# Kernel tuning notes

Hardware: AMD Instinct MI355X
Metric: run time of the kernel (lower is better)

## Reference

```python
import jax, jax.numpy as jnp
import numpy as np

N, NFEAT, NHID, NCLASS, NHEADS = 50000, 512, 256, 64, 8
C1 = NHID // NHEADS  # 32 per-head channels, layer 1
NEG_SLOPE = 0.2


def setup_inputs() -> dict:
    key = jax.random.key(0)
    ks = jax.random.split(key, 10)
    x = jax.random.normal(ks[0], (N, NFEAT), dtype=jnp.float32)
    edge_idx = jax.random.randint(ks[1], (2, 800000), 0, N, dtype=jnp.int64)
    s = 0.05
    return {
        "x": x,
        "edge_idx": edge_idx,
        "W1": jax.random.normal(ks[2], (NFEAT, NHEADS, C1), dtype=jnp.float32) * s,
        "a1_src": jax.random.normal(ks[3], (NHEADS, C1), dtype=jnp.float32) * s,
        "a1_dst": jax.random.normal(ks[4], (NHEADS, C1), dtype=jnp.float32) * s,
        "b1": jnp.zeros((NHID,), dtype=jnp.float32),
        "W2": jax.random.normal(ks[5], (NHID, NHEADS, NCLASS), dtype=jnp.float32) * s,
        "a2_src": jax.random.normal(ks[6], (NHEADS, NCLASS), dtype=jnp.float32) * s,
        "a2_dst": jax.random.normal(ks[7], (NHEADS, NCLASS), dtype=jnp.float32) * s,
        "b2": jnp.zeros((NCLASS,), dtype=jnp.float32),
    }


def gat_conv(x, src, dst, W, a_src, a_dst, b, concat):
    # x: [N, F_in]; W: [F_in, H, C]; a_*: [H, C]; src/dst: [E]
    h = jnp.einsum("nf,fhc->nhc", x, W)             # [N, H, C]
    e_src = jnp.sum(h * a_src, axis=-1)              # [N, H]
    e_dst = jnp.sum(h * a_dst, axis=-1)              # [N, H]
    alpha = e_src[src] + e_dst[dst]                  # [E, H]
    alpha = jnp.where(alpha > 0, alpha, NEG_SLOPE * alpha)  # leaky_relu(0.2)
    # segment softmax over incoming edges of each destination node
    m = jax.ops.segment_max(alpha, dst, num_segments=N)     # [N, H]
    m = jnp.where(jnp.isfinite(m), m, 0.0)
    e = jnp.exp(alpha - m[dst])                      # [E, H]
    z = jax.ops.segment_sum(e, dst, num_segments=N)  # [N, H]
    coef = e / z[dst]                                # [E, H]
    msg = h[src] * coef[:, :, None]                  # [E, H, C]
    out = jax.ops.segment_sum(msg, dst, num_segments=N)  # [N, H, C]
    if concat:
        out = out.reshape(N, -1)
    else:
        out = out.mean(axis=1)
    return out + b


def reference(x, edge_idx, W1, a1_src, a1_dst, b1, W2, a2_src, a2_dst, b2):
    # add self loops (PyG GATConv default)
    loop = jnp.arange(N, dtype=edge_idx.dtype)
    src = jnp.concatenate([edge_idx[0], loop])
    dst = jnp.concatenate([edge_idx[1], loop])
    h = gat_conv(x, src, dst, W1, a1_src, a1_dst, b1, concat=True)   # [N, NHID]
    h = jax.nn.relu(h)
    # dropout inactive (eval mode)
    out = gat_conv(h, src, dst, W2, a2_src, a2_dst, b2, concat=False)  # [N, NCLASS]
    return jax.nn.log_softmax(out, axis=1)
```

## Files before the change

kernel.cpp:

```cpp
#include <hip/hip_runtime.h>
#include <math.h>

#define NN 50000
#define NF 512
#define NHID 256
#define NCLASS 64
#define NHEADS 8

typedef __attribute__((ext_vector_type(8))) short bf16x8;
typedef __attribute__((ext_vector_type(4))) float f32x4;
typedef __attribute__((ext_vector_type(4))) unsigned int u32x4;
typedef __attribute__((ext_vector_type(2))) unsigned int u32x2;

static __device__ __forceinline__ unsigned short f2bf(float f) {
  unsigned int u = __float_as_uint(f);
  unsigned int r = (u + 0x7fffu + ((u >> 16) & 1u)) >> 16;
  return (unsigned short)r;
}
static __device__ __forceinline__ float bf2f(unsigned short u) {
  return __uint_as_float(((unsigned int)u) << 16);
}
static __device__ __forceinline__ float2 bfpair(unsigned int u) {
  return make_float2(__uint_as_float(u << 16), __uint_as_float(u & 0xffff0000u));
}

static __device__ __forceinline__ u32x4 gld128(const void* p) {
  u32x4 r;
  asm volatile("global_load_dwordx4 %0, %1, off"
               : "=v"(r) : "v"((unsigned long long)p));
  return r;
}
static __device__ __forceinline__ u32x2 gld64(const void* p) {
  u32x2 r;
  asm volatile("global_load_dwordx2 %0, %1, off"
               : "=v"(r) : "v"((unsigned long long)p));
  return r;
}
static __device__ __forceinline__ int gld32i(const void* p) {
  int r;
  asm volatile("global_load_dword %0, %1, off"
               : "=v"(r) : "v"((unsigned long long)p));
  return r;
}
static __device__ __forceinline__ float gld32f(const void* p) {
  float r;
  asm volatile("global_load_dword %0, %1, off"
               : "=v"(r) : "v"((unsigned long long)p));
  return r;
}
#define VMCNT0()                                        \
  do {                                                  \
    asm volatile("s_waitcnt vmcnt(0)" ::: "memory");    \
    __builtin_amdgcn_sched_barrier(0);                  \
  } while (0)

__global__ void k_init_deg(int* deg) {
  int i = blockIdx.x * blockDim.x + threadIdx.x;
  if (i < NN) deg[i] = 1;
}

__global__ void k_count(const int* __restrict__ dst, int E0, int* deg) {
  int i = blockIdx.x * blockDim.x + threadIdx.x;
  if (i < E0) atomicAdd(&deg[dst[i]], 1);
}

__global__ __launch_bounds__(1024) void k_scan(const int* __restrict__ deg, int* offs,
                                               int* cursor) {
  __shared__ int wbase[16];
  __shared__ int srun;
  int tid = threadIdx.x;
  int lane = tid & 63;
  int wv = tid >> 6;
  if (tid == 0) srun = 0;
  __syncthreads();
  for (int base = 0; base < NN; base += 4096) {
    int i = base + tid * 4;
    int4 v;
    if (i + 3 < NN) {
      v = *(const int4*)(deg + i);
    } else {
      v.x = (i + 0 < NN) ? deg[i + 0] : 0;
      v.y = (i + 1 < NN) ? deg[i + 1] : 0;
      v.z = (i + 2 < NN) ? deg[i + 2] : 0;
      v.w = (i + 3 < NN) ? deg[i + 3] : 0;
    }
    int tot = v.x + v.y + v.z + v.w;
    int s = tot;
    #pragma unroll
    for (int o = 1; o < 64; o <<= 1) {
      int t = __shfl_up(s, o);
      if (lane >= o) s += t;
    }
    if (lane == 63) wbase[wv] = s;
    __syncthreads();
    if (tid == 0) {
      int run = srun;
      #pragma unroll
      for (int w2 = 0; w2 < 16; w2++) {
        int t = wbase[w2];
        wbase[w2] = run;
        run += t;
      }
      srun = run;
    }
    __syncthreads();
    int p = wbase[wv] + s - tot;
    if (i + 0 < NN) { offs[i + 0] = p; cursor[i + 0] = p; p += v.x; }
    if (i + 1 < NN) { offs[i + 1] = p; cursor[i + 1] = p; p += v.y; }
    if (i + 2 < NN) { offs[i + 2] = p; cursor[i + 2] = p; p += v.z; }
    if (i + 3 < NN) { offs[i + 3] = p; cursor[i + 3] = p; }
  }
  __syncthreads();
  if (tid == 0) offs[NN] = srun;
}

__global__ void k_scatter(const int* __restrict__ src, const int* __restrict__ dst,
                          int E0, int* cursor, int* __restrict__ nbr) {
  int i = blockIdx.x * blockDim.x + threadIdx.x;
  if (i < E0) {
    int pos = atomicAdd(&cursor[dst[i]], 1);
    nbr[pos] = src[i];
  } else if (i < E0 + NN) {
    int v = i - E0;
    int pos = atomicAdd(&cursor[v], 1);
    nbr[pos] = v;
  }
}

__global__ void k_cast4(const float* __restrict__ in, unsigned short* __restrict__ out,
                        int n4) {
  int i = blockIdx.x * blockDim.x + threadIdx.x;
  if (i >= n4) return;
  float4 v = *(const float4*)(in + (size_t)i * 4);
  ushort4 o;
  o.x = f2bf(v.x); o.y = f2bf(v.y); o.z = f2bf(v.z); o.w = f2bf(v.w);
  *(ushort4*)(out + (size_t)i * 4) = o;
}

__global__ void k_castWt(const float* __restrict__ W, unsigned short* __restrict__ Wt,
                         int K, int cols) {
  int i = blockIdx.x * blockDim.x + threadIdx.x;
  if (i >= K * cols) return;
  int k = i / cols, c = i % cols;
  Wt[(size_t)c * K + k] = f2bf(W[i]);
}

__global__ void k_castWt_perm(const float* __restrict__ W, unsigned short* __restrict__ Wt,
                              int K) {
  int i = blockIdx.x * blockDim.x + threadIdx.x;
  if (i >= K * NHEADS * NCLASS) return;
  int k = i / (NHEADS * NCLASS);
  int rem = i % (NHEADS * NCLASS);
  int h = rem / NCLASS, c = rem % NCLASS;
  Wt[(size_t)(c * NHEADS + h) * K + k] = f2bf(W[i]);
}

__global__ __launch_bounds__(256) void k_gemm_bf(const unsigned short* __restrict__ A,
                                                 const unsigned short* __restrict__ Bt,
                                                 unsigned short* __restrict__ C,
                                                 int rows, int K, int cols) {
  __shared__ unsigned short Bs[256 * 40];
  int t = threadIdx.x;
  int wave = t >> 6, lane = t & 63;
  int quad = lane >> 4, sixt = lane & 15;
  int rb = blockIdx.x * 64 + (wave >> 1) * 32;
  int cw = (wave & 1) * 128;
  int cbw = blockIdx.y * 256 + cw;
  int r0 = rb + sixt, r1 = rb + 16 + sixt;
  const unsigned short* Ap0 = A + (size_t)(r0 < rows ? r0 : 0) * K + quad * 8;
  const unsigned short* Ap1 = A + (size_t)(r1 < rows ? r1 : 0) * K + quad * 8;
  const unsigned short* Bg = Bt + (size_t)(blockIdx.y * 256 + (t >> 2)) * K + (t & 3) * 8;
  const size_t BgStep = (size_t)64 * K;
  char* BsW = (char*)Bs + (t >> 2) * 80 + (t & 3) * 16;
  f32x4 acc0[8] = {}, acc1[8] = {};
  for (int k0 = 0; k0 < K; k0 += 32) {
    uint4 v0 = *(const uint4*)(Bg + k0);
    uint4 v1 = *(const uint4*)(Bg + BgStep + k0);
    uint4 v2 = *(const uint4*)(Bg + 2 * BgStep + k0);
    uint4 v3 = *(const uint4*)(Bg + 3 * BgStep + k0);
    bf16x8 a0 = *(const bf16x8*)(Ap0 + k0);
    bf16x8 a1 = *(const bf16x8*)(Ap1 + k0);
    *(uint4*)(BsW) = v0;
    *(uint4*)(BsW + 64 * 80) = v1;
    *(uint4*)(BsW + 128 * 80) = v2;
    *(uint4*)(BsW + 192 * 80) = v3;
    __syncthreads();
    #pragma unroll
    for (int g = 0; g < 8; g++) {
      bf16x8 b = *(const bf16x8*)((const char*)Bs + (cw + g * 16 + sixt) * 80 + quad * 16);
      acc0[g] = __builtin_amdgcn_mfma_f32_16x16x32_bf16(a0, b, acc0[g], 0, 0, 0);
      acc1[g] = __builtin_amdgcn_mfma_f32_16x16x32_bf16(a1, b, acc1[g], 0, 0, 0);
    }
    __syncthreads();
  }
  #pragma unroll
  for (int r = 0; r < 4; r++) {
    int row = rb + quad * 4 + r;
    if (row < rows) {
      unsigned short* out = C + (size_t)row * cols + cbw + sixt;
      #pragma unroll
      for (int g = 0; g < 8; g++) out[g * 16] = f2bf(acc0[g][r]);
    }
    int row2 = row + 16;
    if (row2 < rows) {
      unsigned short* out = C + (size_t)row2 * cols + cbw + sixt;
      #pragma unroll
      for (int g = 0; g < 8; g++) out[g * 16] = f2bf(acc1[g][r]);
    }
  }
}

template <int C>
__global__ void k_escore_c(const unsigned short* __restrict__ h,
                           const float* __restrict__ asr, const float* __restrict__ ads,
                           float* __restrict__ es, float* __restrict__ ed) {
  int idx = blockIdx.x * blockDim.x + threadIdx.x;
  if (idx >= NN * NHEADS) return;
  int hd = idx & 7;
  const unsigned short* row = h + (size_t)idx * C;
  float s = 0.f, d = 0.f;
  #pragma unroll
  for (int c8 = 0; c8 < C / 8; c8++) {
    uint4 raw = *(const uint4*)(row + c8 * 8);
    float2 p0 = bfpair(raw.x), p1 = bfpair(raw.y), p2 = bfpair(raw.z), p3 = bfpair(raw.w);
    const float* as_ = asr + hd * C + c8 * 8;
    const float* ad_ = ads + hd * C + c8 * 8;
    s += p0.x * as_[0] + p0.y * as_[1] + p1.x * as_[2] + p1.y * as_[3] +
         p2.x * as_[4] + p2.y * as_[5] + p3.x * as_[6] + p3.y * as_[7];
    d += p0.x * ad_[0] + p0.y * ad_[1] + p1.x * ad_[2] + p1.y * ad_[3] +
         p2.x * ad_[4] + p2.y * ad_[5] + p3.x * ad_[6] + p3.y * ad_[7];
  }
  es[idx] = s;
  ed[idx] = d;
}

__global__ void k_escore_p(const unsigned short* __restrict__ h,
                           const float* __restrict__ asr, const float* __restrict__ ads,
                           float* __restrict__ es, float* __restrict__ ed) {
  int idx = blockIdx.x * blockDim.x + threadIdx.x;
  if (idx >= NN * NHEADS) return;
  int hd = idx & 7;
  int n = idx >> 3;
  const unsigned short* row = h + (size_t)n * (NHEADS * NCLASS) + hd;
  float s = 0.f, d = 0.f;
  #pragma unroll
  for (int c = 0; c < NCLASS; c++) {
    float v = bf2f(row[c * NHEADS]);
    s += v * asr[hd * NCLASS + c];
    d += v * ads[hd * NCLASS + c];
  }
  es[idx] = s;
  ed[idx] = d;
}

__global__ __launch_bounds__(256) void k_agg1f(const int* __restrict__ offs,
                                               const int* __restrict__ nbr,
                                               const unsigned short* __restrict__ h1,
                                               const float* __restrict__ es,
                                               const float* __restrict__ ed,
                                               const float* __restrict__ b1,
                                               unsigned short* __restrict__ out) {
  int node = blockIdx.x * 4 + (threadIdx.x >> 6);
  if (node >= NN) return;
  int lane = threadIdx.x & 63;
  int h = lane & 7;
  int sub = lane >> 3;
  int col = lane << 2;
  int beg = offs[node], end = offs[node + 1];
  float edst = ed[node * NHEADS + h];
  int kb = beg;
  int iA = kb + (lane & 7); if (iA > end - 1) iA = end - 1;
  int vt = gld32i(nbr + iA);
  int vtN = 0;
  if (kb + 8 < end) {
    int iB = kb + 8 + (lane & 7); if (iB > end - 1) iB = end - 1;
    vtN = gld32i(nbr + iB);
  }
  VMCNT0();
  int se[8];
  #pragma unroll
  for (int e = 0; e < 8; e++) se[e] = __shfl(vt, e);
  float esv;
  {
    int sv = __shfl(vt, sub);
    esv = gld32f(es + (size_t)sv * NHEADS + h);
  }
  VMCNT0();
  float m = -1e30f, z = 0.f;
  float4 acc = make_float4(0.f, 0.f, 0.f, 0.f);
  while (true) {
    int cnt = end - kb; if (cnt > 8) cnt = 8;
    u32x2 r[8];
    #pragma unroll
    for (int e = 0; e < 8; e++)
      if (e < cnt) r[e] = gld64(h1 + (size_t)se[e] * NHID + col);
    bool more = kb + 8 < end, more2 = kb + 16 < end;
    int vt2 = 0;
    if (more2) {
      int iC = kb + 16 + (lane & 7); if (iC > end - 1) iC = end - 1;
      vt2 = gld32i(nbr + iC);
    }
    float esvN = 0.f;
    if (more) {
      int svN = __shfl(vtN, sub);
      esvN = gld32f(es + (size_t)svN * NHEADS + h);
    }
    float ar = esv + edst;
    ar = (ar > 0.f) ? ar : 0.2f * ar;
    float a = (kb + sub < end) ? ar : -1e30f;
    float gm = a;
    #pragma unroll
    for (int o = 8; o < 64; o <<= 1) gm = fmaxf(gm, __shfl_xor(gm, o));
    float mn = fmaxf(m, gm);
    float ee = __expf(a - mn);
    float zg = ee;
    #pragma unroll
    for (int o = 8; o < 64; o <<= 1) zg += __shfl_xor(zg, o);
    float sc = __expf(m - mn);
    z = z * sc + zg;
    m = mn;
    VMCNT0();
    float sch = __shfl(sc, sub);
    acc.x *= sch; acc.y *= sch; acc.z *= sch; acc.w *= sch;
    #pragma unroll
    for (int e = 0; e < 8; e++) {
      if (e < cnt) {
        float ce = __shfl(ee, e * 8 + sub);
        float2 p0 = bfpair(r[e][0]), p1 = bfpair(r[e][1]);
        acc.x += ce * p0.x;
        acc.y += ce * p0.y;
        acc.z += ce * p1.x;
        acc.w += ce * p1.y;
      }
    }
    if (!more) break;
    kb += 8;
    #pragma unroll
    for (int e = 0; e < 8; e++) se[e] = __shfl(vtN, e);
    esv = esvN;
    vtN = vt2;
  }
  float inv = 1.f / z;
  float ivh = __shfl(inv, sub);
  ushort4 o;
  o.x = f2bf(fmaxf(acc.x * ivh + b1[col + 0], 0.f));
  o.y = f2bf(fmaxf(acc.y * ivh + b1[col + 1], 0.f));
  o.z = f2bf(fmaxf(acc.z * ivh + b1[col + 2], 0.f));
  o.w = f2bf(fmaxf(acc.w * ivh + b1[col + 3], 0.f));
  *(ushort4*)(out + (size_t)node * NHID + col) = o;
}

__global__ __launch_bounds__(256) void k_agg2f(const int* __restrict__ offs,
                                               const int* __restrict__ nbr,
                                               const unsigned short* __restrict__ h2,
                                               const float* __restrict__ es,
                                               const float* __restrict__ ed,
                                               const float* __restrict__ b2,
                                               float* __restrict__ out) {
  __shared__ __align__(16) float cs[4][64];
  int wv = threadIdx.x >> 6;
  int node = blockIdx.x * 4 + wv;
  if (node >= NN) return;
  int lane = threadIdx.x & 63;
  int h = lane & 7;
  int sub = lane >> 3;
  int beg = offs[node], end = offs[node + 1];
  float edst = ed[node * NHEADS + h];
  int kb = beg;
  int iA = kb + (lane & 7); if (iA > end - 1) iA = end - 1;
  int vt = gld32i(nbr + iA);
  int vtN = 0;
  if (kb + 8 < end) {
    int iB = kb + 8 + (lane & 7); if (iB > end - 1) iB = end - 1;
    vtN = gld32i(nbr + iB);
  }
  VMCNT0();
  int se[8];
  #pragma unroll
  for (int e = 0; e < 8; e++) se[e] = __shfl(vt, e);
  float esv;
  {
    int sv = __shfl(vt, sub);
    esv = gld32f(es + (size_t)sv * NHEADS + h);
  }
  VMCNT0();
  float m = -1e30f, z = 0.f;
  float acc[8] = {};
  while (true) {
    int cnt = end - kb; if (cnt > 8) cnt = 8;
    u32x4 r[8];
    #pragma unroll
    for (int e = 0; e < 8; e++)
      if (e < cnt) r[e] = gld128(h2 + (size_t)se[e] * (NHEADS * NCLASS) + (lane << 3));
    bool more = kb + 8 < end, more2 = kb + 16 < end;
    int vt2 = 0;
    if (more2) {
      int iC = kb + 16 + (lane & 7); if (iC > end - 1) iC = end - 1;
      vt2 = gld32i(nbr + iC);
    }
    float esvN = 0.f;
    if (more) {
      int svN = __shfl(vtN, sub);
      esvN = gld32f(es + (size_t)svN * NHEADS + h);
    }
    float ar = esv + edst;
    ar = (ar > 0.f) ? ar : 0.2f * ar;
    float a = (kb + sub < end) ? ar : -1e30f;
    float gm = a;
    #pragma unroll
    for (int o = 8; o < 64; o <<= 1) gm = fmaxf(gm, __shfl_xor(gm, o));
    float mn = fmaxf(m, gm);
    float ee = __expf(a - mn);
    float zg = ee;
    #pragma unroll
    for (int o = 8; o < 64; o <<= 1) zg += __shfl_xor(zg, o);
    float sc = __expf(m - mn);
    z = z * sc + zg;
    m = mn;
    cs[wv][lane] = ee;
    VMCNT0();
    #pragma unroll
    for (int hh = 0; hh < 8; hh++) acc[hh] *= __shfl(sc, hh);
    #pragma unroll
    for (int e = 0; e < 8; e++) {
      if (e < cnt) {
        float4 cA = *(const float4*)&cs[wv][e * 8];
        float4 cB = *(const float4*)&cs[wv][e * 8 + 4];
        float2 p0 = bfpair(r[e][0]), p1 = bfpair(r[e][1]), p2 = bfpair(r[e][2]),
               p3 = bfpair(r[e][3]);
        acc[0] += cA.x * p0.x;
        acc[1] += cA.y * p0.y;
        acc[2] += cA.z * p1.x;
        acc[3] += cA.w * p1.y;
        acc[4] += cB.x * p2.x;
        acc[5] += cB.y * p2.y;
        acc[6] += cB.z * p3.x;
        acc[7] += cB.w * p3.y;
      }
    }
    if (!more) break;
    kb += 8;
    #pragma unroll
    for (int e = 0; e < 8; e++) se[e] = __shfl(vtN, e);
    esv = esvN;
    vtN = vt2;
  }
  float inv = 1.f / z;
  float val = 0.f;
  #pragma unroll
  for (int hh = 0; hh < 8; hh++) val += acc[hh] * __shfl(inv, hh);
  val = val * 0.125f + b2[lane];
  float mx = val;
  #pragma unroll
  for (int o = 32; o > 0; o >>= 1) mx = fmaxf(mx, __shfl_xor(mx, o));
  float ex = __expf(val - mx);
  float sm = ex;
  #pragma unroll
  for (int o = 32; o > 0; o >>= 1) sm += __shfl_xor(sm, o);
  out[(size_t)node * NCLASS + lane] = val - mx - __logf(sm);
}

extern "C" void kernel_launch(void* const* d_in, const int* in_sizes, int n_in,
                              void* d_out, int out_size, void* d_ws, size_t ws_size,
                              hipStream_t stream) {
  const float* x   = (const float*)d_in[0];
  const int* eidx  = (const int*)d_in[1];
  const float* W1  = (const float*)d_in[2];
  const float* a1s = (const float*)d_in[3];
  const float* a1d = (const float*)d_in[4];
  const float* b1  = (const float*)d_in[5];
  const float* W2  = (const float*)d_in[6];
  const float* a2s = (const float*)d_in[7];
  const float* a2d = (const float*)d_in[8];
  const float* b2  = (const float*)d_in[9];
  const int E0 = in_sizes[1] / 2;
  const int* esrc = eidx;
  const int* edst = eidx + E0;
  const int E = E0 + NN;

  char* w = (char*)d_ws;
  auto carve = [&](size_t bytes) {
    void* p = (void*)w;
    w += (bytes + 255) & ~(size_t)255;
    return p;
  };
  int* deg      = (int*)carve((size_t)NN * 4);
  int* offs     = (int*)carve((size_t)(NN + 1) * 4);
  int* cursor   = (int*)carve((size_t)NN * 4);
  int* nbr      = (int*)carve((size_t)E * 4);
  float* es1    = (float*)carve((size_t)NN * NHEADS * 4);
  float* ed1    = (float*)carve((size_t)NN * NHEADS * 4);
  unsigned short* xbf   = (unsigned short*)carve((size_t)NN * NF * 2);
  unsigned short* W1t   = (unsigned short*)carve((size_t)NF * NHID * 2);
  unsigned short* W2t   = (unsigned short*)carve((size_t)NHID * NHEADS * NCLASS * 2);
  unsigned short* h1b   = (unsigned short*)carve((size_t)NN * NHID * 2);
  unsigned short* out1b = (unsigned short*)carve((size_t)NN * NHID * 2);
  unsigned short* h2b   = (unsigned short*)carve((size_t)NN * NHEADS * NCLASS * 2);

  k_init_deg<<<(NN + 255) / 256, 256, 0, stream>>>(deg);
  k_count<<<(E0 + 255) / 256, 256, 0, stream>>>(edst, E0, deg);
  k_scan<<<1, 1024, 0, stream>>>(deg, offs, cursor);
  k_scatter<<<(E0 + NN + 255) / 256, 256, 0, stream>>>(esrc, edst, E0, cursor, nbr);

  k_cast4<<<(NN * NF / 4 + 255) / 256, 256, 0, stream>>>(x, xbf, NN * NF / 4);
  k_castWt<<<(NF * NHID + 255) / 256, 256, 0, stream>>>(W1, W1t, NF, NHID);
  k_castWt_perm<<<(NHID * NHEADS * NCLASS + 255) / 256, 256, 0, stream>>>(W2, W2t, NHID);

  k_gemm_bf<<<dim3((NN + 63) / 64, NHID / 256), 256, 0, stream>>>(xbf, W1t, h1b,
                                                                  NN, NF, NHID);
  k_escore_c<32><<<(NN * NHEADS + 255) / 256, 256, 0, stream>>>(h1b, a1s, a1d, es1, ed1);
  k_agg1f<<<(NN + 3) / 4, 256, 0, stream>>>(offs, nbr, h1b, es1, ed1, b1, out1b);

  k_gemm_bf<<<dim3((NN + 63) / 64, (NHEADS * NCLASS) / 256), 256, 0, stream>>>(
      out1b, W2t, h2b, NN, NHID, NHEADS * NCLASS);
  k_escore_p<<<(NN * NHEADS + 255) / 256, 256, 0, stream>>>(h2b, a2s, a2d, es1, ed1);
  k_agg2f<<<(NN + 3) / 4, 256, 0, stream>>>(offs, nbr, h2b, es1, ed1, b2, (float*)d_out);
}
```

Baseline: 607.1 us.

## Double-buffer neighbor feature gathers in GAT aggregation kernels with partial vmcnt waits

Both aggregation kernels now issue the gathers for the next 8-edge chunk into a second register buffer before computing the current chunk. Waits use partial `s_waitcnt vmcnt(8)` instead of full drains, so feature-row loads overlap the softmax and accumulation math. Index and score prefetch is pushed one chunk further ahead, and the per-edge `cnt` guards are dropped in favour of clamped indices plus zero weights. The cost is higher register pressure from two 8-entry buffers. Counting of in-flight inline-asm loads is fragile: the next score value may be read before its load is covered by a wait.

```diff
diff --git a/kernel.cpp b/kernel.cpp
--- a/kernel.cpp
+++ b/kernel.cpp
@@ -48,10 +48,10 @@
                : "=v"(r) : "v"((unsigned long long)p));
   return r;
 }
-#define VMCNT0()                                        \
-  do {                                                  \
-    asm volatile("s_waitcnt vmcnt(0)" ::: "memory");    \
-    __builtin_amdgcn_sched_barrier(0);                  \
+#define VMWAIT(N)                                              \
+  do {                                                         \
+    asm volatile("s_waitcnt vmcnt(" #N ")" ::: "memory");      \
+    __builtin_amdgcn_sched_barrier(0);                         \
   } while (0)
 
 __global__ void k_init_deg(int* deg) {
@@ -266,44 +266,36 @@
   int h = lane & 7;
   int sub = lane >> 3;
   int col = lane << 2;
-  int beg = offs[node], end = offs[node + 1];
-  float edst = ed[node * NHEADS + h];
+  int beg = gld32i(offs + node);
+  int end = gld32i(offs + node + 1);
+  float edst = gld32f(ed + node * NHEADS + h);
+  VMWAIT(0);
   int kb = beg;
-  int iA = kb + (lane & 7); if (iA > end - 1) iA = end - 1;
-  int vt = gld32i(nbr + iA);
-  int vtN = 0;
-  if (kb + 8 < end) {
-    int iB = kb + 8 + (lane & 7); if (iB > end - 1) iB = end - 1;
-    vtN = gld32i(nbr + iB);
-  }
-  VMCNT0();
-  int se[8];
-  #pragma unroll
-  for (int e = 0; e < 8; e++) se[e] = __shfl(vt, e);
+  int i0 = kb + (lane & 7); if (i0 > end - 1) i0 = end - 1;
+  int vt0 = gld32i(nbr + i0);
+  VMWAIT(0);
+  int vt1 = 0, vt2 = 0;
+  if (kb + 8 < end)  { int i1 = kb + 8 + (lane & 7);  if (i1 > end - 1) i1 = end - 1; vt1 = gld32i(nbr + i1); }
+  if (kb + 16 < end) { int i2 = kb + 16 + (lane & 7); if (i2 > end - 1) i2 = end - 1; vt2 = gld32i(nbr + i2); }
   float esv;
-  {
-    int sv = __shfl(vt, sub);
-    esv = gld32f(es + (size_t)sv * NHEADS + h);
-  }
-  VMCNT0();
+  { int sv = __shfl(vt0, sub); esv = gld32f(es + (size_t)sv * NHEADS + h); }
+  u32x2 rA[8], rB[8];
+  #pragma unroll
+  for (int e = 0; e < 8; e++) {
+    int sv = __shfl(vt0, e);
+    rA[e] = gld64(h1 + (size_t)sv * NHID + col);
+  }
+  VMWAIT(8);
   float m = -1e30f, z = 0.f;
   float4 acc = make_float4(0.f, 0.f, 0.f, 0.f);
-  while (true) {
-    int cnt = end - kb; if (cnt > 8) cnt = 8;
-    u32x2 r[8];
-    #pragma unroll
-    for (int e = 0; e < 8; e++)
-      if (e < cnt) r[e] = gld64(h1 + (size_t)se[e] * NHID + col);
-    bool more = kb + 8 < end, more2 = kb + 16 < end;
-    int vt2 = 0;
-    if (more2) {
-      int iC = kb + 16 + (lane & 7); if (iC > end - 1) iC = end - 1;
-      vt2 = gld32i(nbr + iC);
-    }
-    float esvN = 0.f;
+  auto iterate = [&](u32x2 (&rCur)[8], u32x2 (&rNxt)[8]) -> bool {
+    bool more = kb + 8 < end;
     if (more) {
-      int svN = __shfl(vtN, sub);
-      esvN = gld32f(es + (size_t)svN * NHEADS + h);
+      #pragma unroll
+      for (int e = 0; e < 8; e++) {
+        int sv = __shfl(vt1, e);
+        rNxt[e] = gld64(h1 + (size_t)sv * NHID + col);
+      }
     }
     float ar = esv + edst;
     ar = (ar > 0.f) ? ar : 0.2f * ar;
@@ -319,26 +311,29 @@
     float sc = __expf(m - mn);
     z = z * sc + zg;
     m = mn;
-    VMCNT0();
+    if (more) { VMWAIT(8); } else { VMWAIT(0); }
+    float esvN = 0.f;
+    int vtNew = 0;
+    if (more) { int sv = __shfl(vt1, sub); esvN = gld32f(es + (size_t)sv * NHEADS + h); }
+    if (kb + 24 < end) { int i3 = kb + 24 + (lane & 7); if (i3 > end - 1) i3 = end - 1; vtNew = gld32i(nbr + i3); }
     float sch = __shfl(sc, sub);
     acc.x *= sch; acc.y *= sch; acc.z *= sch; acc.w *= sch;
     #pragma unroll
     for (int e = 0; e < 8; e++) {
-      if (e < cnt) {
-        float ce = __shfl(ee, e * 8 + sub);
-        float2 p0 = bfpair(r[e][0]), p1 = bfpair(r[e][1]);
-        acc.x += ce * p0.x;
-        acc.y += ce * p0.y;
-        acc.z += ce * p1.x;
-        acc.w += ce * p1.y;
-      }
-    }
-    if (!more) break;
+      float ce = __shfl(ee, e * 8 + sub);
+      float2 p0 = bfpair(rCur[e][0]), p1 = bfpair(rCur[e][1]);
+      acc.x += ce * p0.x;
+      acc.y += ce * p0.y;
+      acc.z += ce * p1.x;
+      acc.w += ce * p1.y;
+    }
     kb += 8;
-    #pragma unroll
-    for (int e = 0; e < 8; e++) se[e] = __shfl(vtN, e);
-    esv = esvN;
-    vtN = vt2;
+    vt1 = vt2; vt2 = vtNew; esv = esvN;
+    return more;
+  };
+  while (true) {
+    if (!iterate(rA, rB)) break;
+    if (!iterate(rB, rA)) break;
   }
   float inv = 1.f / z;
   float ivh = __shfl(inv, sub);
@@ -364,44 +359,36 @@
   int lane = threadIdx.x & 63;
   int h = lane & 7;
   int sub = lane >> 3;
-  int beg = offs[node], end = offs[node + 1];
-  float edst = ed[node * NHEADS + h];
+  int beg = gld32i(offs + node);
+  int end = gld32i(offs + node + 1);
+  float edst = gld32f(ed + node * NHEADS + h);
+  VMWAIT(0);
   int kb = beg;
-  int iA = kb + (lane & 7); if (iA > end - 1) iA = end - 1;
-  int vt = gld32i(nbr + iA);
-  int vtN = 0;
-  if (kb + 8 < end) {
-    int iB = kb + 8 + (lane & 7); if (iB > end - 1) iB = end - 1;
-    vtN = gld32i(nbr + iB);
-  }
-  VMCNT0();
-  int se[8];
-  #pragma unroll
-  for (int e = 0; e < 8; e++) se[e] = __shfl(vt, e);
+  int i0 = kb + (lane & 7); if (i0 > end - 1) i0 = end - 1;
+  int vt0 = gld32i(nbr + i0);
+  VMWAIT(0);
+  int vt1 = 0, vt2 = 0;
+  if (kb + 8 < end)  { int i1 = kb + 8 + (lane & 7);  if (i1 > end - 1) i1 = end - 1; vt1 = gld32i(nbr + i1); }
+  if (kb + 16 < end) { int i2 = kb + 16 + (lane & 7); if (i2 > end - 1) i2 = end - 1; vt2 = gld32i(nbr + i2); }
   float esv;
-  {
-    int sv = __shfl(vt, sub);
-    esv = gld32f(es + (size_t)sv * NHEADS + h);
-  }
-  VMCNT0();
+  { int sv = __shfl(vt0, sub); esv = gld32f(es + (size_t)sv * NHEADS + h); }
+  u32x4 rA[8], rB[8];
+  #pragma unroll
+  for (int e = 0; e < 8; e++) {
+    int sv = __shfl(vt0, e);
+    rA[e] = gld128(h2 + (size_t)sv * (NHEADS * NCLASS) + (lane << 3));
+  }
+  VMWAIT(8);
   float m = -1e30f, z = 0.f;
   float acc[8] = {};
-  while (true) {
-    int cnt = end - kb; if (cnt > 8) cnt = 8;
-    u32x4 r[8];
-    #pragma unroll
-    for (int e = 0; e < 8; e++)
-      if (e < cnt) r[e] = gld128(h2 + (size_t)se[e] * (NHEADS * NCLASS) + (lane << 3));
-    bool more = kb + 8 < end, more2 = kb + 16 < end;
-    int vt2 = 0;
-    if (more2) {
-      int iC = kb + 16 + (lane & 7); if (iC > end - 1) iC = end - 1;
-      vt2 = gld32i(nbr + iC);
-    }
-    float esvN = 0.f;
+  auto iterate = [&](u32x4 (&rCur)[8], u32x4 (&rNxt)[8]) -> bool {
+    bool more = kb + 8 < end;
     if (more) {
-      int svN = __shfl(vtN, sub);
-      esvN = gld32f(es + (size_t)svN * NHEADS + h);
+      #pragma unroll
+      for (int e = 0; e < 8; e++) {
+        int sv = __shfl(vt1, e);
+        rNxt[e] = gld128(h2 + (size_t)sv * (NHEADS * NCLASS) + (lane << 3));
+      }
     }
     float ar = esv + edst;
     ar = (ar > 0.f) ? ar : 0.2f * ar;
@@ -418,32 +405,35 @@
     z = z * sc + zg;
     m = mn;
     cs[wv][lane] = ee;
-    VMCNT0();
+    if (more) { VMWAIT(8); } else { VMWAIT(0); }
+    float esvN = 0.f;
+    int vtNew = 0;
+    if (more) { int sv = __shfl(vt1, sub); esvN = gld32f(es + (size_t)sv * NHEADS + h); }
+    if (kb + 24 < end) { int i3 = kb + 24 + (lane & 7); if (i3 > end - 1) i3 = end - 1; vtNew = gld32i(nbr + i3); }
     #pragma unroll
     for (int hh = 0; hh < 8; hh++) acc[hh] *= __shfl(sc, hh);
     #pragma unroll
     for (int e = 0; e < 8; e++) {
-      if (e < cnt) {
-        float4 cA = *(const float4*)&cs[wv][e * 8];
-        float4 cB = *(const float4*)&cs[wv][e * 8 + 4];
-        float2 p0 = bfpair(r[e][0]), p1 = bfpair(r[e][1]), p2 = bfpair(r[e][2]),
-               p3 = bfpair(r[e][3]);
-        acc[0] += cA.x * p0.x;
-        acc[1] += cA.y * p0.y;
-        acc[2] += cA.z * p1.x;
-        acc[3] += cA.w * p1.y;
-        acc[4] += cB.x * p2.x;
-        acc[5] += cB.y * p2.y;
-        acc[6] += cB.z * p3.x;
-        acc[7] += cB.w * p3.y;
-      }
-    }
-    if (!more) break;
+      float4 cA = *(const float4*)&cs[wv][e * 8];
+      float4 cB = *(const float4*)&cs[wv][e * 8 + 4];
+      float2 p0 = bfpair(rCur[e][0]), p1 = bfpair(rCur[e][1]),
+             p2 = bfpair(rCur[e][2]), p3 = bfpair(rCur[e][3]);
+      acc[0] += cA.x * p0.x;
+      acc[1] += cA.y * p0.y;
+      acc[2] += cA.z * p1.x;
+      acc[3] += cA.w * p1.y;
+      acc[4] += cB.x * p2.x;
+      acc[5] += cB.y * p2.y;
+      acc[6] += cB.z * p3.x;
+      acc[7] += cB.w * p3.y;
+    }
     kb += 8;
-    #pragma unroll
-    for (int e = 0; e < 8; e++) se[e] = __shfl(vtN, e);
-    esv = esvN;
-    vtN = vt2;
+    vt1 = vt2; vt2 = vtNew; esv = esvN;
+    return more;
+  };
+  while (true) {
+    if (!iterate(rA, rB)) break;
+    if (!iterate(rB, rA)) break;
   }
   float inv = 1.f / z;
   float val = 0.f;
```

New measurement: 628.4 us. 3.5% more time.
